# Kernel tuning notes

Measured on AMD Instinct MI355X. Metric: run time of the kernel, lower is better.

## Reference

```python
import jax, jax.numpy as jnp
import numpy as np

B, CH, CW, H, FH, FW = 32, 16, 16, 8, 4, 4
NQ = 64
NK = CH * FH * CW * FW  # 4096
D_IN, D_V, D_MODEL = 512, 64, 512


def setup_inputs() -> dict:
    key = jax.random.key(0)
    k1, k2, k3, k4, k5 = jax.random.split(key, 5)
    att12 = jax.random.uniform(k1, (B, CH, CW, H, FH, FW), dtype=jnp.float32)
    att3 = jax.random.uniform(k2, (B, H, NQ, CH * CW), dtype=jnp.float32)
    values = jax.random.normal(k3, (B, NK, D_IN), dtype=jnp.float32)
    # Learned params (xavier-ish scale)
    W_v = jax.random.normal(k4, (H * D_V, D_IN), dtype=jnp.float32) * (1.0 / np.sqrt(D_IN))
    b_v = jnp.zeros((H * D_V,), dtype=jnp.float32)
    W_o = jax.random.normal(k5, (D_MODEL, H * D_V), dtype=jnp.float32) * (1.0 / np.sqrt(H * D_V))
    b_o = jnp.zeros((D_MODEL,), dtype=jnp.float32)
    return {"att12": att12, "att3": att3, "values": values,
            "W_v": W_v, "b_v": b_v, "W_o": W_o, "b_o": b_o}


def reference(att12, att3, values, W_v, b_v, W_o, b_o):
    b_s, h, nq, _ = att3.shape
    ch = cw = CH
    fh, fw = att12.shape[-2:]
    nk = values.shape[1]
    d_v = W_v.shape[0] // h
    # v: [b, h, nk, d_v]
    v = (values @ W_v.T + b_v).reshape(b_s, nk, h, d_v).transpose(0, 2, 1, 3)
    # att12 -> [b, h, 1, ch, cw, fh, fw]
    a12 = jnp.transpose(att12, (0, 3, 1, 2, 4, 5))[:, :, None]
    # att3 -> [b, h, nq, ch, cw, 1, 1]
    a3 = att3.reshape(b_s, h, nq, ch, cw, 1, 1)
    # broadcast multiply, then interleave to key order (ch, fh, cw, fw)
    att = (a12 * a3).transpose(0, 1, 2, 3, 5, 4, 6).reshape(b_s, h, nq, nk)
    att = jax.nn.softmax(att, axis=-1)
    out = jnp.einsum('bhqk,bhkd->bhqd', att, v)
    out = out.transpose(0, 2, 1, 3).reshape(b_s, nq, h * d_v)
    return out @ W_o.T + b_o
```

## Files before the change

kernel.cpp:

```cpp
#include <hip/hip_runtime.h>

typedef short bf16x8 __attribute__((ext_vector_type(8)));
typedef short bf16x4 __attribute__((ext_vector_type(4)));
typedef float f32x4 __attribute__((ext_vector_type(4)));
typedef unsigned int u32x2 __attribute__((ext_vector_type(2)));
typedef unsigned int u32x4 __attribute__((ext_vector_type(4)));

__device__ __forceinline__ unsigned short f2bf(float f) {
  union { float f; unsigned u; } v; v.f = f;
  unsigned r = v.u + 0x7fffu + ((v.u >> 16) & 1u);
  return (unsigned short)(r >> 16);
}

__device__ __forceinline__ unsigned int pk2(float a, float b) {
  union { float f; unsigned u; } x, y; x.f = a; y.f = b;
  return __builtin_amdgcn_perm(y.u + 0x8000u, x.u + 0x8000u, 0x07060302u);
}

__device__ __forceinline__ void gld_lds16(const void* g, void* l) {
  __builtin_amdgcn_global_load_lds(
      (const __attribute__((address_space(1))) void*)g,
      (__attribute__((address_space(3))) void*)l, 16, 0, 0);
}

__global__ __launch_bounds__(256) void prep(const float* __restrict__ W_v,
                                            const float* __restrict__ W_o,
                                            const float* __restrict__ b_v,
                                            const float* __restrict__ b_o,
                                            unsigned short* __restrict__ Wvb,
                                            unsigned short* __restrict__ Wob,
                                            float* __restrict__ bias2) {
  int bid = blockIdx.x;
  if (bid < 512) {
    const float* in = (bid < 256) ? W_v : W_o;
    unsigned short* out = (bid < 256) ? Wvb : Wob;
    long i = (long)((bid & 255) * 256 + threadIdx.x) * 4;
    f32x4 d = *(const f32x4*)(in + i);
    u32x2 w; w[0] = pk2(d[0], d[1]); w[1] = pk2(d[2], d[3]);
    *(u32x2*)(out + i) = w;
  } else {
    int e = (bid - 512) * 256 + threadIdx.x;
    const float* wrow = W_o + (long)e * 512;
    float s = 0.f;
#pragma unroll 4
    for (int d = 0; d < 512; d += 4) {
      f32x4 w = *(const f32x4*)(wrow + d);
      f32x4 bv = *(const f32x4*)(b_v + d);
      s += w[0] * bv[0] + w[1] * bv[1] + w[2] * bv[2] + w[3] * bv[3];
    }
    bias2[e] = s + b_o[e];
  }
}

__global__ __launch_bounds__(256, 2) void vt_gemm(
    const unsigned short* __restrict__ Wvb, const float* __restrict__ V,
    unsigned short* __restrict__ vT) {
  const int t = threadIdx.x, lane = t & 63, wave = t >> 6;
  const int n0 = blockIdx.x * 128;
  const int m0 = blockIdx.y * 256;
  const int b = blockIdx.z;
  const float* Vb = V + (long)b * (4096L * 512) + (long)n0 * 512;

  __shared__ __align__(16) unsigned short As[2][256 * 32];
  __shared__ __align__(16) unsigned short Bs[2][128 * 32];

  const int wm = (wave >> 1) * 128, wn = (wave & 1) * 64;
  const int l16 = lane & 15, quad = lane >> 4;
  const int brow0 = t >> 3, bc4 = (t & 7) * 4;

  f32x4 breg[4];
  auto loadB = [&](int k0) {
#pragma unroll
    for (int j = 0; j < 4; ++j)
      breg[j] = *(const f32x4*)(Vb + (long)(brow0 + 32 * j) * 512 + k0 + bc4);
  };
  auto asyncA = [&](int k0, int buf) {
#pragma unroll
    for (int s = 0; s < 4; ++s) {
      int li = s * 256 + t;
      int row = li >> 2, kq = (li & 3) * 8;
      gld_lds16(Wvb + (long)(m0 + row) * 512 + k0 + kq,
                (char*)&As[buf][0] + (s * 256 + wave * 64) * 16);
    }
  };

  f32x4 acc[8][4];
#pragma unroll
  for (int i = 0; i < 8; ++i)
#pragma unroll
    for (int j = 0; j < 4; ++j) acc[i][j] = (f32x4){0.f, 0.f, 0.f, 0.f};

  asyncA(0, 0);
  loadB(0);

  for (int r = 0; r < 16; ++r) {
    const int buf = r & 1;
#pragma unroll
    for (int j = 0; j < 4; ++j) {
      u32x2 w;
      w[0] = pk2(breg[j][0], breg[j][1]);
      w[1] = pk2(breg[j][2], breg[j][3]);
      *(u32x2*)(&Bs[buf][(brow0 + 32 * j) * 32 + bc4]) = w;
    }
    __syncthreads();
    if (r < 15) {
      loadB((r + 1) * 32);
      asyncA((r + 1) * 32, buf ^ 1);
    }
    bf16x8 bfv[4];
#pragma unroll
    for (int j = 0; j < 4; ++j)
      bfv[j] = *(const bf16x8*)(&Bs[buf][(wn + j * 16 + l16) * 32 + quad * 8]);
#pragma unroll
    for (int i = 0; i < 8; ++i) {
      bf16x8 af = *(const bf16x8*)(&As[buf][(wm + i * 16 + l16) * 32 + quad * 8]);
#pragma unroll
      for (int j = 0; j < 4; ++j)
        acc[i][j] = __builtin_amdgcn_mfma_f32_16x16x32_bf16(af, bfv[j], acc[i][j], 0, 0, 0);
    }
  }

  unsigned short* o = vT + (long)b * 2097152;
#pragma unroll
  for (int i = 0; i < 8; ++i)
#pragma unroll
    for (int j = 0; j < 4; ++j) {
      int col = n0 + wn + j * 16 + l16;
#pragma unroll
      for (int r = 0; r < 4; ++r) {
        int row = m0 + wm + i * 16 + quad * 4 + r;
        o[(long)row * 4096 + col] = f2bf(acc[i][j][r]);
      }
    }
}

__global__ __launch_bounds__(256, 2) void o_gemm(
    const float* __restrict__ att12, const float* __restrict__ att3,
    const unsigned short* __restrict__ vT, unsigned short* __restrict__ U) {
  const int bh = blockIdx.x;
  const int b = bh >> 3, h = bh & 7;
  const int t = threadIdx.x, lane = t & 63, wave = t >> 6;

  __shared__ __align__(16) unsigned short As[2][4 * 64 * 40];
  __shared__ __align__(16) unsigned short Bs[3][4 * 64 * 32];
  __shared__ float Ored[64 * 68];
  __shared__ float Zl[4][64];
  __shared__ float rZa[64];

  const unsigned short* vTb = vT + (long)b * 2097152 + (long)h * 64 * 4096;
  const int gq = t & 63, gw = t >> 6;
  const float* a3row = att3 + ((long)bh * 64 + gq) * 256;
  const float* a12b = att12 + (long)b * 32768 + h * 16;
  const int l16 = lane & 15, quad = lane >> 4;

  f32x4 acc[4][4];
#pragma unroll
  for (int i = 0; i < 4; ++i)
#pragma unroll
    for (int j = 0; j < 4; ++j) acc[i][j] = (f32x4){0.f, 0.f, 0.f, 0.f};
  float zacc = 0.f;

  unsigned int pk[16];
  auto genexp = [&](int r) {
    int kbase = gw * 1024 + r * 32;
    int ch = kbase >> 8, fh = (kbase >> 6) & 3, cw0 = (kbase >> 2) & 15;
    f32x4 y0 = *(const f32x4*)(a3row + ch * 16 + cw0);
    f32x4 y1 = *(const f32x4*)(a3row + ch * 16 + cw0 + 4);
    const float* ap = a12b + ch * 2048 + cw0 * 128 + fh * 4;
#pragma unroll
    for (int cw = 0; cw < 8; ++cw) {
      float y = (cw < 4) ? y0[cw] : y1[cw - 4];
      f32x4 x = *(const f32x4*)(ap + cw * 128);
      float e0 = __expf(x[0] * y), e1 = __expf(x[1] * y);
      float e2 = __expf(x[2] * y), e3 = __expf(x[3] * y);
      zacc += (e0 + e1) + (e2 + e3);
      pk[cw * 2] = pk2(e0, e1);
      pk[cw * 2 + 1] = pk2(e2, e3);
    }
  };
  auto asyncB = [&](int rr, int slot) {
    const int rc = (rr < 32) ? rr : 0;
#pragma unroll
    for (int s = 0; s < 4; ++s) {
      int row = t >> 2, kq = (t & 3) * 8;
      int kk = s * 1024 + rc * 32 + kq;
      gld_lds16(vTb + (long)row * 4096 + kk, (char*)&Bs[slot][0] + s * 4096 + wave * 1024);
    }
  };

  asyncB(0, 0);
  asyncB(1, 1);
  genexp(0);

  int slotR = 0, slotW = 2;
  for (int r = 0; r < 32; ++r) {
    const int abuf = r & 1;
    {
      unsigned short* dst = &As[abuf][gw * 2560 + gq * 40];
#pragma unroll
      for (int g = 0; g < 4; ++g)
        *(u32x4*)(dst + g * 8) = (u32x4){pk[g * 4], pk[g * 4 + 1], pk[g * 4 + 2], pk[g * 4 + 3]};
    }
    asm volatile("s_waitcnt vmcnt(4) lgkmcnt(0)" ::: "memory");
    __builtin_amdgcn_s_barrier();
    asm volatile("" ::: "memory");
    asyncB(r + 2, slotW);
    asm volatile("" ::: "memory");
    bf16x8 af[4], bfv[4];
#pragma unroll
    for (int i = 0; i < 4; ++i)
      af[i] = *(const bf16x8*)(&As[abuf][wave * 2560 + (i * 16 + l16) * 40 + quad * 8]);
#pragma unroll
    for (int j = 0; j < 4; ++j)
      bfv[j] = *(const bf16x8*)(&Bs[slotR][wave * 2048 + (j * 16 + l16) * 32 + quad * 8]);
#pragma unroll
    for (int i = 0; i < 4; ++i)
#pragma unroll
      for (int j = 0; j < 4; ++j)
        acc[i][j] = __builtin_amdgcn_mfma_f32_16x16x32_bf16(af[i], bfv[j], acc[i][j], 0, 0, 0);
    if (r < 31) genexp(r + 1);
    slotR = (slotR == 2) ? 0 : slotR + 1;
    slotW = (slotW == 2) ? 0 : slotW + 1;
  }
  asm volatile("s_waitcnt vmcnt(0)" ::: "memory");

  Zl[gw][gq] = zacc;
  __syncthreads();
  if (t < 64) rZa[t] = 1.0f / (Zl[0][t] + Zl[1][t] + Zl[2][t] + Zl[3][t]);
#pragma unroll
  for (int w = 0; w < 4; ++w) {
    if (wave == w) {
#pragma unroll
      for (int i = 0; i < 4; ++i)
#pragma unroll
        for (int j = 0; j < 4; ++j) {
          int col = j * 16 + l16;
#pragma unroll
          for (int rr = 0; rr < 4; ++rr) {
            int row = i * 16 + quad * 4 + rr;
            if (w == 0) Ored[row * 68 + col] = acc[i][j][rr];
            else Ored[row * 68 + col] += acc[i][j][rr];
          }
        }
    }
    __syncthreads();
  }
  {
    int q = t >> 2, dv0 = (t & 3) * 16;
    float rz = rZa[q];
    unsigned short* up = U + ((long)(b * 64 + q)) * 512 + h * 64 + dv0;
    u32x4 o0, o1;
#pragma unroll
    for (int j = 0; j < 4; ++j)
      o0[j] = pk2(Ored[q * 68 + dv0 + 2 * j] * rz, Ored[q * 68 + dv0 + 2 * j + 1] * rz);
#pragma unroll
    for (int j = 0; j < 4; ++j)
      o1[j] = pk2(Ored[q * 68 + dv0 + 8 + 2 * j] * rz, Ored[q * 68 + dv0 + 9 + 2 * j] * rz);
    *(u32x4*)(up) = o0;
    *(u32x4*)(up + 8) = o1;
  }
}

template <int BM, int BN>
__global__ __launch_bounds__(256, 2) void gemm_bt(
    const unsigned short* __restrict__ A, const unsigned short* __restrict__ Bt,
    float* __restrict__ C, const float* __restrict__ bias,
    int K, int lda, int ldb, int ldc) {
  constexpr int BK = 32;
  const int t = threadIdx.x;
  const int lane = t & 63;
  const int wave = t >> 6;
  const int m0 = blockIdx.y * BM;
  const int n0 = blockIdx.x * BN;

  A += (long)m0 * lda;
  Bt += (long)n0 * ldb;

  __shared__ __align__(16) unsigned short As[3][BM * BK];
  __shared__ __align__(16) unsigned short Bs[3][BN * BK];

  constexpr int TM = BM / 32;
  constexpr int TN = BN / 32;
  const int wm = (wave >> 1) * (BM / 2);
  const int wn = (wave & 1) * (BN / 2);
  const int l16 = lane & 15;
  const int quad = lane >> 4;

  f32x4 acc[TM][TN];
#pragma unroll
  for (int i = 0; i < TM; ++i)
#pragma unroll
    for (int j = 0; j < TN; ++j) acc[i][j] = (f32x4){0.f, 0.f, 0.f, 0.f};

  constexpr int ASHOT = (BM * 4) / 256;
  constexpr int BSHOT = (BN * 4) / 256;
  const int NIT = K / BK;

  auto stage = [&](int rr, int slot) {
    const int k0 = ((rr < NIT) ? rr : 0) * BK;
#pragma unroll
    for (int s = 0; s < ASHOT; ++s) {
      int li = s * 256 + t;
      int row = li >> 2, kq = (li & 3) * 8;
      gld_lds16(A + (long)row * lda + k0 + kq,
                (char*)&As[slot][0] + (s * 256 + wave * 64) * 16);
    }
#pragma unroll
    for (int s = 0; s < BSHOT; ++s) {
      int li = s * 256 + t;
      int row = li >> 2, kq = (li & 3) * 8;
      gld_lds16(Bt + (long)row * ldb + k0 + kq,
                (char*)&Bs[slot][0] + (s * 256 + wave * 64) * 16);
    }
  };

  stage(0, 0);
  stage(1, 1);

  int slotR = 0, slotW = 2;
  for (int r = 0; r < NIT; ++r) {
    asm volatile("s_waitcnt vmcnt(2)" ::: "memory");
    __builtin_amdgcn_s_barrier();
    asm volatile("" ::: "memory");
    stage(r + 2, slotW);
    asm volatile("" ::: "memory");
    bf16x8 af[TM], bfv[TN];
#pragma unroll
    for (int i = 0; i < TM; ++i)
      af[i] = *(const bf16x8*)(&As[slotR][(wm + i * 16 + l16) * BK + quad * 8]);
#pragma unroll
    for (int j = 0; j < TN; ++j)
      bfv[j] = *(const bf16x8*)(&Bs[slotR][(wn + j * 16 + l16) * BK + quad * 8]);
#pragma unroll
    for (int i = 0; i < TM; ++i)
#pragma unroll
      for (int j = 0; j < TN; ++j)
        acc[i][j] = __builtin_amdgcn_mfma_f32_16x16x32_bf16(af[i], bfv[j], acc[i][j], 0, 0, 0);
    slotR = (slotR == 2) ? 0 : slotR + 1;
    slotW = (slotW == 2) ? 0 : slotW + 1;
  }
  asm volatile("s_waitcnt vmcnt(0)" ::: "memory");

#pragma unroll
  for (int i = 0; i < TM; ++i) {
#pragma unroll
    for (int j = 0; j < TN; ++j) {
      int col = wn + j * 16 + l16;
#pragma unroll
      for (int r = 0; r < 4; ++r) {
        int row = wm + i * 16 + quad * 4 + r;
        C[(long)(m0 + row) * ldc + (n0 + col)] = acc[i][j][r] + bias[n0 + col];
      }
    }
  }
}

extern "C" void kernel_launch(void* const* d_in, const int* in_sizes, int n_in,
                              void* d_out, int out_size, void* d_ws, size_t ws_size,
                              hipStream_t stream) {
  const float* att12 = (const float*)d_in[0];
  const float* att3  = (const float*)d_in[1];
  const float* values = (const float*)d_in[2];
  const float* W_v = (const float*)d_in[3];
  const float* b_v = (const float*)d_in[4];
  const float* W_o = (const float*)d_in[5];
  const float* b_o = (const float*)d_in[6];
  float* out = (float*)d_out;

  char* ws = (char*)d_ws;
  unsigned short* vT    = (unsigned short*)(ws);
  unsigned short* U     = (unsigned short*)(ws + 134217728L);
  unsigned short* Wvb   = (unsigned short*)(ws + 136314880L);
  unsigned short* Wob   = (unsigned short*)(ws + 136839168L);
  float*          bias2 = (float*)(ws + 137363456L);

  prep<<<dim3(514), dim3(256), 0, stream>>>(W_v, W_o, b_v, b_o, Wvb, Wob, bias2);

  vt_gemm<<<dim3(32, 2, 32), dim3(256), 0, stream>>>(Wvb, values, vT);

  o_gemm<<<dim3(256), dim3(256), 0, stream>>>(att12, att3, vT, U);

  gemm_bt<64, 64><<<dim3(8, 32), dim3(256), 0, stream>>>(
      U, Wob, out, bias2, 512, 512, 512, 512);

  (void)in_sizes; (void)n_in; (void)out_size; (void)ws_size;
}
```

Measured before the change: 531.2 us.

## Reassociate attention before value projection and fold W_v into output weights

Applies the softmax attention directly to the raw input values per head, then multiplies by a precomputed combined matrix W_o·W_v in a single K=4096 GEMM. This removes the large bf16 projected-value intermediate and its write/read traffic, as well as a separate kernel. In exchange, the exponentials are recomputed for each 64-column tile of values, the final GEMM has a much longer K, and bf16 rounding of the fused weights changes numerics.

```diff
diff --git a/kernel.cpp b/kernel.cpp
--- a/kernel.cpp
+++ b/kernel.cpp
@@ -1,8 +1,8 @@
 #include <hip/hip_runtime.h>
 
 typedef short bf16x8 __attribute__((ext_vector_type(8)));
-typedef short bf16x4 __attribute__((ext_vector_type(4)));
 typedef float f32x4 __attribute__((ext_vector_type(4)));
+typedef float f32x2 __attribute__((ext_vector_type(2)));
 typedef unsigned int u32x2 __attribute__((ext_vector_type(2)));
 typedef unsigned int u32x4 __attribute__((ext_vector_type(4)));
 
@@ -23,23 +23,40 @@
       (__attribute__((address_space(3))) void*)l, 16, 0, 0);
 }
 
-__global__ __launch_bounds__(256) void prep(const float* __restrict__ W_v,
-                                            const float* __restrict__ W_o,
-                                            const float* __restrict__ b_v,
-                                            const float* __restrict__ b_o,
-                                            unsigned short* __restrict__ Wvb,
-                                            unsigned short* __restrict__ Wob,
-                                            float* __restrict__ bias2) {
-  int bid = blockIdx.x;
-  if (bid < 512) {
-    const float* in = (bid < 256) ? W_v : W_o;
-    unsigned short* out = (bid < 256) ? Wvb : Wob;
-    long i = (long)((bid & 255) * 256 + threadIdx.x) * 4;
-    f32x4 d = *(const f32x4*)(in + i);
-    u32x2 w; w[0] = pk2(d[0], d[1]); w[1] = pk2(d[2], d[3]);
-    *(u32x2*)(out + i) = w;
+__global__ __launch_bounds__(256) void prep2(const float* __restrict__ W_v,
+                                             const float* __restrict__ W_o,
+                                             const float* __restrict__ b_v,
+                                             const float* __restrict__ b_o,
+                                             unsigned short* __restrict__ Gtb,
+                                             float* __restrict__ bias2) {
+  const int bid = blockIdx.x, t = threadIdx.x;
+  if (bid < 128) {
+    const int h = bid >> 4, et = bid & 15;
+    const int e = et * 32 + (t >> 3);
+    const int cs = (t & 7) * 64;
+    const float* wv = W_v + (long)(h * 64) * 512 + cs;
+    const float* wo = W_o + (long)e * 512 + h * 64;
+    f32x4 a[16];
+#pragma unroll
+    for (int q = 0; q < 16; ++q) a[q] = (f32x4){0.f, 0.f, 0.f, 0.f};
+    for (int dv = 0; dv < 64; ++dv) {
+      float ws = wo[dv];
+      const f32x4* row = (const f32x4*)(wv + (long)dv * 512);
+#pragma unroll
+      for (int q = 0; q < 16; ++q) a[q] += row[q] * ws;
+    }
+    unsigned short* g = Gtb + (long)e * 4096 + h * 512 + cs;
+#pragma unroll
+    for (int q = 0; q < 16; q += 2) {
+      u32x4 wb;
+      wb[0] = pk2(a[q][0], a[q][1]);
+      wb[1] = pk2(a[q][2], a[q][3]);
+      wb[2] = pk2(a[q + 1][0], a[q + 1][1]);
+      wb[3] = pk2(a[q + 1][2], a[q + 1][3]);
+      *(u32x4*)(g + q * 4) = wb;
+    }
   } else {
-    int e = (bid - 512) * 256 + threadIdx.x;
+    const int e = (bid - 128) * 256 + t;
     const float* wrow = W_o + (long)e * 512;
     float s = 0.f;
 #pragma unroll 4
@@ -52,212 +69,120 @@
   }
 }
 
-__global__ __launch_bounds__(256, 2) void vt_gemm(
-    const unsigned short* __restrict__ Wvb, const float* __restrict__ V,
-    unsigned short* __restrict__ vT) {
-  const int t = threadIdx.x, lane = t & 63, wave = t >> 6;
-  const int n0 = blockIdx.x * 128;
-  const int m0 = blockIdx.y * 256;
-  const int b = blockIdx.z;
-  const float* Vb = V + (long)b * (4096L * 512) + (long)n0 * 512;
-
-  __shared__ __align__(16) unsigned short As[2][256 * 32];
-  __shared__ __align__(16) unsigned short Bs[2][128 * 32];
-
-  const int wm = (wave >> 1) * 128, wn = (wave & 1) * 64;
+__global__ __launch_bounds__(512, 2) void y_gemm(
+    const float* __restrict__ att12, const float* __restrict__ att3,
+    const float* __restrict__ values, unsigned short* __restrict__ Y) {
+  const int nt = blockIdx.x, b = blockIdx.y;
+  const int c0 = nt * 64;
+  const int t = threadIdx.x, lane = t & 63, w = t >> 6;
   const int l16 = lane & 15, quad = lane >> 4;
-  const int brow0 = t >> 3, bc4 = (t & 7) * 4;
-
-  f32x4 breg[4];
-  auto loadB = [&](int k0) {
+
+  __shared__ __align__(16) unsigned short Bs[2][64 * 40];
+  __shared__ float Zs[512];
+
+  const float* Vb   = values + (long)b * (4096L * 512) + c0;
+  const float* a12b = att12 + (long)b * 32768 + w * 16;
+  const float* a3b  = att3 + (long)(b * 8 + w) * 64 * 256;
+
+  const bool stager = (t < 256);
+  const int kp = t >> 4;
+  const int cq = t & 15;
+
+  f32x4 acc[4][4];
+#pragma unroll
+  for (int i = 0; i < 4; ++i)
+#pragma unroll
+    for (int j = 0; j < 4; ++j) acc[i][j] = (f32x4){0.f, 0.f, 0.f, 0.f};
+  float z[4] = {0.f, 0.f, 0.f, 0.f};
+  f32x2 a3p0[4], a3p1[4];
+  f32x4 v0r, v1r;
+
+  auto loadV = [&](int k0) {
+    const float* p = Vb + (long)(k0 + 2 * kp) * 512 + 4 * cq;
+    v0r = *(const f32x4*)(p);
+    v1r = *(const f32x4*)(p + 512);
+  };
+  auto packV = [&](int buf) {
+#pragma unroll
+    for (int i = 0; i < 4; ++i) {
+      unsigned pw = pk2(v0r[i], v1r[i]);
+      *(unsigned*)(&Bs[buf][(4 * cq + i) * 40 + 2 * kp]) = pw;
+    }
+  };
+  auto loadA3 = [&](int ch) {
+#pragma unroll
+    for (int i = 0; i < 4; ++i) {
+      const float* ap = a3b + (long)(i * 16 + l16) * 256 + ch * 16 + quad * 2;
+      a3p0[i] = *(const f32x2*)(ap);
+      a3p1[i] = *(const f32x2*)(ap + 8);
+    }
+  };
+
+  auto step = [&](int r, int buf, int sel) {
+    const int ch = r >> 3, fh = (r >> 1) & 3;
+    const int cwb = sel * 8 + quad * 2;
+    const float* xp = a12b + ch * 2048 + cwb * 128 + fh * 4;
+    f32x4 x0 = *(const f32x4*)(xp);
+    f32x4 x1 = *(const f32x4*)(xp + 128);
+    bf16x8 af[4];
+#pragma unroll
+    for (int i = 0; i < 4; ++i) {
+      f32x2 y = sel ? a3p1[i] : a3p0[i];
+      float e0 = __expf(x0[0] * y[0]), e1 = __expf(x0[1] * y[0]);
+      float e2 = __expf(x0[2] * y[0]), e3 = __expf(x0[3] * y[0]);
+      float e4 = __expf(x1[0] * y[1]), e5 = __expf(x1[1] * y[1]);
+      float e6 = __expf(x1[2] * y[1]), e7 = __expf(x1[3] * y[1]);
+      z[i] += (e0 + e1) + (e2 + e3) + ((e4 + e5) + (e6 + e7));
+      u32x4 ab;
+      ab[0] = pk2(e0, e1); ab[1] = pk2(e2, e3);
+      ab[2] = pk2(e4, e5); ab[3] = pk2(e6, e7);
+      af[i] = *(bf16x8*)&ab;
+    }
+    __syncthreads();
+    if (stager && r < 127) loadV((r + 1) * 32);
+    bf16x8 bfv[4];
 #pragma unroll
     for (int j = 0; j < 4; ++j)
-      breg[j] = *(const f32x4*)(Vb + (long)(brow0 + 32 * j) * 512 + k0 + bc4);
-  };
-  auto asyncA = [&](int k0, int buf) {
-#pragma unroll
-    for (int s = 0; s < 4; ++s) {
-      int li = s * 256 + t;
-      int row = li >> 2, kq = (li & 3) * 8;
-      gld_lds16(Wvb + (long)(m0 + row) * 512 + k0 + kq,
-                (char*)&As[buf][0] + (s * 256 + wave * 64) * 16);
-    }
-  };
-
-  f32x4 acc[8][4];
-#pragma unroll
-  for (int i = 0; i < 8; ++i)
-#pragma unroll
-    for (int j = 0; j < 4; ++j) acc[i][j] = (f32x4){0.f, 0.f, 0.f, 0.f};
-
-  asyncA(0, 0);
-  loadB(0);
-
-  for (int r = 0; r < 16; ++r) {
-    const int buf = r & 1;
-#pragma unroll
-    for (int j = 0; j < 4; ++j) {
-      u32x2 w;
-      w[0] = pk2(breg[j][0], breg[j][1]);
-      w[1] = pk2(breg[j][2], breg[j][3]);
-      *(u32x2*)(&Bs[buf][(brow0 + 32 * j) * 32 + bc4]) = w;
-    }
-    __syncthreads();
-    if (r < 15) {
-      loadB((r + 1) * 32);
-      asyncA((r + 1) * 32, buf ^ 1);
-    }
-    bf16x8 bfv[4];
-#pragma unroll
-    for (int j = 0; j < 4; ++j)
-      bfv[j] = *(const bf16x8*)(&Bs[buf][(wn + j * 16 + l16) * 32 + quad * 8]);
-#pragma unroll
-    for (int i = 0; i < 8; ++i) {
-      bf16x8 af = *(const bf16x8*)(&As[buf][(wm + i * 16 + l16) * 32 + quad * 8]);
-#pragma unroll
-      for (int j = 0; j < 4; ++j)
-        acc[i][j] = __builtin_amdgcn_mfma_f32_16x16x32_bf16(af, bfv[j], acc[i][j], 0, 0, 0);
-    }
-  }
-
-  unsigned short* o = vT + (long)b * 2097152;
-#pragma unroll
-  for (int i = 0; i < 8; ++i)
-#pragma unroll
-    for (int j = 0; j < 4; ++j) {
-      int col = n0 + wn + j * 16 + l16;
-#pragma unroll
-      for (int r = 0; r < 4; ++r) {
-        int row = m0 + wm + i * 16 + quad * 4 + r;
-        o[(long)row * 4096 + col] = f2bf(acc[i][j][r]);
-      }
-    }
-}
-
-__global__ __launch_bounds__(256, 2) void o_gemm(
-    const float* __restrict__ att12, const float* __restrict__ att3,
-    const unsigned short* __restrict__ vT, unsigned short* __restrict__ U) {
-  const int bh = blockIdx.x;
-  const int b = bh >> 3, h = bh & 7;
-  const int t = threadIdx.x, lane = t & 63, wave = t >> 6;
-
-  __shared__ __align__(16) unsigned short As[2][4 * 64 * 40];
-  __shared__ __align__(16) unsigned short Bs[3][4 * 64 * 32];
-  __shared__ float Ored[64 * 68];
-  __shared__ float Zl[4][64];
-  __shared__ float rZa[64];
-
-  const unsigned short* vTb = vT + (long)b * 2097152 + (long)h * 64 * 4096;
-  const int gq = t & 63, gw = t >> 6;
-  const float* a3row = att3 + ((long)bh * 64 + gq) * 256;
-  const float* a12b = att12 + (long)b * 32768 + h * 16;
-  const int l16 = lane & 15, quad = lane >> 4;
-
-  f32x4 acc[4][4];
-#pragma unroll
-  for (int i = 0; i < 4; ++i)
-#pragma unroll
-    for (int j = 0; j < 4; ++j) acc[i][j] = (f32x4){0.f, 0.f, 0.f, 0.f};
-  float zacc = 0.f;
-
-  unsigned int pk[16];
-  auto genexp = [&](int r) {
-    int kbase = gw * 1024 + r * 32;
-    int ch = kbase >> 8, fh = (kbase >> 6) & 3, cw0 = (kbase >> 2) & 15;
-    f32x4 y0 = *(const f32x4*)(a3row + ch * 16 + cw0);
-    f32x4 y1 = *(const f32x4*)(a3row + ch * 16 + cw0 + 4);
-    const float* ap = a12b + ch * 2048 + cw0 * 128 + fh * 4;
-#pragma unroll
-    for (int cw = 0; cw < 8; ++cw) {
-      float y = (cw < 4) ? y0[cw] : y1[cw - 4];
-      f32x4 x = *(const f32x4*)(ap + cw * 128);
-      float e0 = __expf(x[0] * y), e1 = __expf(x[1] * y);
-      float e2 = __expf(x[2] * y), e3 = __expf(x[3] * y);
-      zacc += (e0 + e1) + (e2 + e3);
-      pk[cw * 2] = pk2(e0, e1);
-      pk[cw * 2 + 1] = pk2(e2, e3);
-    }
-  };
-  auto asyncB = [&](int rr, int slot) {
-    const int rc = (rr < 32) ? rr : 0;
-#pragma unroll
-    for (int s = 0; s < 4; ++s) {
-      int row = t >> 2, kq = (t & 3) * 8;
-      int kk = s * 1024 + rc * 32 + kq;
-      gld_lds16(vTb + (long)row * 4096 + kk, (char*)&Bs[slot][0] + s * 4096 + wave * 1024);
-    }
-  };
-
-  asyncB(0, 0);
-  asyncB(1, 1);
-  genexp(0);
-
-  int slotR = 0, slotW = 2;
-  for (int r = 0; r < 32; ++r) {
-    const int abuf = r & 1;
-    {
-      unsigned short* dst = &As[abuf][gw * 2560 + gq * 40];
-#pragma unroll
-      for (int g = 0; g < 4; ++g)
-        *(u32x4*)(dst + g * 8) = (u32x4){pk[g * 4], pk[g * 4 + 1], pk[g * 4 + 2], pk[g * 4 + 3]};
-    }
-    asm volatile("s_waitcnt vmcnt(4) lgkmcnt(0)" ::: "memory");
-    __builtin_amdgcn_s_barrier();
-    asm volatile("" ::: "memory");
-    asyncB(r + 2, slotW);
-    asm volatile("" ::: "memory");
-    bf16x8 af[4], bfv[4];
-#pragma unroll
-    for (int i = 0; i < 4; ++i)
-      af[i] = *(const bf16x8*)(&As[abuf][wave * 2560 + (i * 16 + l16) * 40 + quad * 8]);
-#pragma unroll
-    for (int j = 0; j < 4; ++j)
-      bfv[j] = *(const bf16x8*)(&Bs[slotR][wave * 2048 + (j * 16 + l16) * 32 + quad * 8]);
+      bfv[j] = *(const bf16x8*)(&Bs[buf][(j * 16 + l16) * 40 + quad * 8]);
 #pragma unroll
     for (int i = 0; i < 4; ++i)
 #pragma unroll
       for (int j = 0; j < 4; ++j)
         acc[i][j] = __builtin_amdgcn_mfma_f32_16x16x32_bf16(af[i], bfv[j], acc[i][j], 0, 0, 0);
-    if (r < 31) genexp(r + 1);
-    slotR = (slotR == 2) ? 0 : slotR + 1;
-    slotW = (slotW == 2) ? 0 : slotW + 1;
-  }
-  asm volatile("s_waitcnt vmcnt(0)" ::: "memory");
-
-  Zl[gw][gq] = zacc;
+  };
+
+  if (stager) loadV(0);
+  loadA3(0);
+  for (int rr = 0; rr < 128; rr += 2) {
+    if ((rr & 7) == 0 && rr) loadA3(rr >> 3);
+    if (stager) packV(0);
+    step(rr, 0, 0);
+    if (stager) packV(1);
+    step(rr + 1, 1, 1);
+  }
+
+#pragma unroll
+  for (int i = 0; i < 4; ++i) {
+    z[i] += __shfl_xor(z[i], 16);
+    z[i] += __shfl_xor(z[i], 32);
+  }
+  if (quad == 0) {
+#pragma unroll
+    for (int i = 0; i < 4; ++i) Zs[w * 64 + i * 16 + l16] = z[i];
+  }
   __syncthreads();
-  if (t < 64) rZa[t] = 1.0f / (Zl[0][t] + Zl[1][t] + Zl[2][t] + Zl[3][t]);
-#pragma unroll
-  for (int w = 0; w < 4; ++w) {
-    if (wave == w) {
-#pragma unroll
-      for (int i = 0; i < 4; ++i)
-#pragma unroll
-        for (int j = 0; j < 4; ++j) {
-          int col = j * 16 + l16;
-#pragma unroll
-          for (int rr = 0; rr < 4; ++rr) {
-            int row = i * 16 + quad * 4 + rr;
-            if (w == 0) Ored[row * 68 + col] = acc[i][j][rr];
-            else Ored[row * 68 + col] += acc[i][j][rr];
-          }
-        }
-    }
-    __syncthreads();
-  }
-  {
-    int q = t >> 2, dv0 = (t & 3) * 16;
-    float rz = rZa[q];
-    unsigned short* up = U + ((long)(b * 64 + q)) * 512 + h * 64 + dv0;
-    u32x4 o0, o1;
-#pragma unroll
-    for (int j = 0; j < 4; ++j)
-      o0[j] = pk2(Ored[q * 68 + dv0 + 2 * j] * rz, Ored[q * 68 + dv0 + 2 * j + 1] * rz);
-#pragma unroll
-    for (int j = 0; j < 4; ++j)
-      o1[j] = pk2(Ored[q * 68 + dv0 + 8 + 2 * j] * rz, Ored[q * 68 + dv0 + 9 + 2 * j] * rz);
-    *(u32x4*)(up) = o0;
-    *(u32x4*)(up + 8) = o1;
+
+  unsigned short* Yb = Y + (long)b * 64 * 4096 + (long)w * 512 + c0;
+#pragma unroll
+  for (int i = 0; i < 4; ++i) {
+#pragma unroll
+    for (int r2 = 0; r2 < 4; ++r2) {
+      const int q = i * 16 + quad * 4 + r2;
+      const float rz = 1.0f / Zs[w * 64 + q];
+#pragma unroll
+      for (int j = 0; j < 4; ++j)
+        Yb[(long)q * 4096 + j * 16 + l16] = f2bf(acc[i][j][r2] * rz);
+    }
   }
 }
 
@@ -368,20 +293,16 @@
   float* out = (float*)d_out;
 
   char* ws = (char*)d_ws;
-  unsigned short* vT    = (unsigned short*)(ws);
-  unsigned short* U     = (unsigned short*)(ws + 134217728L);
-  unsigned short* Wvb   = (unsigned short*)(ws + 136314880L);
-  unsigned short* Wob   = (unsigned short*)(ws + 136839168L);
-  float*          bias2 = (float*)(ws + 137363456L);
-
-  prep<<<dim3(514), dim3(256), 0, stream>>>(W_v, W_o, b_v, b_o, Wvb, Wob, bias2);
-
-  vt_gemm<<<dim3(32, 2, 32), dim3(256), 0, stream>>>(Wvb, values, vT);
-
-  o_gemm<<<dim3(256), dim3(256), 0, stream>>>(att12, att3, vT, U);
+  unsigned short* Y     = (unsigned short*)(ws);
+  unsigned short* Gtb   = (unsigned short*)(ws + 16777216L);
+  float*          bias2 = (float*)(ws + 20971520L);
+
+  prep2<<<dim3(130), dim3(256), 0, stream>>>(W_v, W_o, b_v, b_o, Gtb, bias2);
+
+  y_gemm<<<dim3(8, 32), dim3(512), 0, stream>>>(att12, att3, values, Y);
 
   gemm_bt<64, 64><<<dim3(8, 32), dim3(256), 0, stream>>>(
-      U, Wob, out, bias2, 512, 512, 512, 512);
+      Y, Gtb, out, bias2, 4096, 4096, 4096, 512);
 
   (void)in_sizes; (void)n_in; (void)out_size; (void)ws_size;
 }
```

Result: slower. 681.1 us (+28.2%).
